# Kernel optimization log

Measured on AMD Instinct MI355X. Metric: run time of the kernel, lower is better.

## Reference

```python
import jax, jax.numpy as jnp
import numpy as np

B, S, D, H, HD = 2, 2048, 768, 12, 64


def setup_inputs() -> dict:
    key = jax.random.key(0)
    ks = jax.random.split(key, 8)
    w = lambda k, shp: jax.random.normal(k, shp, dtype=jnp.float32) * 0.02
    return {
        "hidden_states": jax.random.normal(ks[0], (B, S, D), dtype=jnp.float32),
        "Wq": w(ks[1], (D, D)), "bq": jnp.zeros((D,), jnp.float32),
        "Wk": w(ks[2], (D, D)), "bk": jnp.zeros((D,), jnp.float32),
        "Wv": w(ks[3], (D, D)), "bv": jnp.zeros((D,), jnp.float32),
        # hedgehog feature maps are initialized to identity in the module
        "Wfq": jnp.eye(HD, dtype=jnp.float32) + w(ks[4], (HD, HD)),
        "bfq": jnp.zeros((HD,), jnp.float32),
        "Wfk": jnp.eye(HD, dtype=jnp.float32) + w(ks[5], (HD, HD)),
        "bfk": jnp.zeros((HD,), jnp.float32),
    }


def _heads(x):
    # [B,S,D] -> [B,H,S,HD]
    return x.reshape(B, S, H, HD).transpose(0, 2, 1, 3)


def _feature_map(x, Wf, bf):
    # exp / exp(-x) hedgehog map: [B,H,S,HD] -> [B,H,S,2*HD]
    y = jnp.einsum('bhsd,ed->bhse', x, Wf) + bf
    return jnp.concatenate([jnp.exp(y), jnp.exp(-y)], axis=-1)


def reference(hidden_states, Wq, bq, Wk, bk, Wv, bv, Wfq, bfq, Wfk, bfk):
    h = hidden_states
    q = _heads(h @ Wq.T + bq)   # [B,H,S,HD]
    k = _heads(h @ Wk.T + bk)
    v = _heads(h @ Wv.T + bv)

    # frozen base (softmax) attention producing outputs + true_attns
    scale = 1.0 / np.sqrt(HD).astype(np.float32)
    scores = jnp.einsum('bhmd,bhnd->bhmn', q, k) * scale
    true_attns = jax.nn.softmax(scores, axis=-1)
    out = jnp.einsum('bhmn,bhnd->bhmd', true_attns, v)
    outputs = out.transpose(0, 2, 1, 3).reshape(B, S, D)

    # hedgehog predicted attention: quadratic linear attention
    fq = _feature_map(q, Wfq, bfq)  # [B,H,S,2*HD]
    fk = _feature_map(k, Wfk, bfk)
    qk = jnp.einsum('bhmd,bhnd->bhmn', fq, fk)
    pred_attns = qk / qk.sum(axis=-1, keepdims=True)

    return outputs, pred_attns, true_attns
```

## Files before the change

kernel.cpp:

```cpp
#include <hip/hip_runtime.h>
#include <math.h>

namespace {

constexpr int kB = 2, kS = 2048, kD = 768, kH = 12, kHD = 64, kF = 128, kBH = kB * kH;

typedef __attribute__((ext_vector_type(8))) short short8;
typedef __attribute__((ext_vector_type(4))) short short4v;
typedef __attribute__((ext_vector_type(4))) float f32x4;

__device__ __forceinline__ ushort f2bf(float x) {
    union { float f; unsigned u; } v; v.f = x;
    return (ushort)((v.u + 0x7fffu + ((v.u >> 16) & 1u)) >> 16);
}
__device__ __forceinline__ float bf2f(ushort u) {
    union { unsigned u; float f; } v; v.u = ((unsigned)u) << 16; return v.f;
}

__device__ __forceinline__ void gload16(const ushort* g, void* lds) {
    __builtin_amdgcn_global_load_lds(
        (const __attribute__((address_space(1))) void*)g,
        (__attribute__((address_space(3))) void*)lds, 16, 0, 0);
}

__device__ __forceinline__ void gstage64x64(ushort* ldsBase, const ushort* g,
                                            size_t strideElems, int w, int lane) {
    #pragma unroll
    for (int j = 0; j < 2; ++j) {
        const int row = 16 * w + 8 * j + (lane >> 3);
        const int chunk = lane & 7;
        const ushort* gp = g + (size_t)row * strideElems + ((chunk ^ (row & 7)) * 8);
        void* lp = (char*)ldsBase + (16 * w + 8 * j) * 128;
        gload16(gp, lp);
    }
}
__device__ __forceinline__ void gstageA128(ushort* ldsBase, const ushort* g,
                                           size_t strideElems, int w, int lane) {
    #pragma unroll
    for (int j = 0; j < 4; ++j) {
        const int row = 32 * w + 8 * j + (lane >> 3);
        const int chunk = lane & 7;
        const ushort* gp = g + (size_t)row * strideElems + ((chunk ^ (row & 7)) * 8);
        void* lp = (char*)ldsBase + (32 * w + 8 * j) * 128;
        gload16(gp, lp);
    }
}

__device__ __forceinline__ void gstage8x64(ushort* ldsBase, const ushort* g,
                                           size_t strideElems, int w, int lane) {
    const int row = 8 * w + (lane >> 3);
    const int chunk = lane & 7;
    gload16(g + (size_t)row * strideElems + ((chunk ^ (row & 7)) * 8),
            (char*)ldsBase + 8 * w * 128);
}
__device__ __forceinline__ void gstage8x128(ushort* ldsBase, const ushort* g,
                                            int w, int lane) {
    #pragma unroll
    for (int j = 0; j < 2; ++j) {
        const int row = 8 * w + 4 * j + (lane >> 4);
        const int chunk = lane & 15;
        gload16(g + (size_t)row * kF + ((chunk ^ (row & 7)) * 8),
                (char*)ldsBase + (8 * w + 4 * j) * 256);
    }
}

__global__ __launch_bounds__(256) void cast_kernel(
    const float* __restrict__ s0, const float* __restrict__ s1,
    const float* __restrict__ s2, const float* __restrict__ s3,
    ushort* __restrict__ d0, ushort* __restrict__ d1,
    ushort* __restrict__ d2, ushort* __restrict__ d3)
{
    const int seg = blockIdx.y;
    const float* src = seg == 0 ? s0 : seg == 1 ? s1 : seg == 2 ? s2 : s3;
    ushort* dst      = seg == 0 ? d0 : seg == 1 ? d1 : seg == 2 ? d2 : d3;
    const int n4 = (seg == 0 ? kB * kS * kD : kD * kD) / 4;
    for (int i = blockIdx.x * 256 + threadIdx.x; i < n4; i += gridDim.x * 256) {
        float4 v = *(const float4*)&src[(size_t)i * 4];
        short4v o;
        o[0] = (short)f2bf(v.x); o[1] = (short)f2bf(v.y);
        o[2] = (short)f2bf(v.z); o[3] = (short)f2bf(v.w);
        *(short4v*)&dst[(size_t)i * 4] = o;
    }
}

__global__ __launch_bounds__(256) void qkv_mfma_kernel(
    const ushort* __restrict__ hb,
    const ushort* __restrict__ Wqb, const ushort* __restrict__ Wkb,
    const ushort* __restrict__ Wvb,
    const float* __restrict__ bq, const float* __restrict__ bk,
    const float* __restrict__ bv,
    const float* __restrict__ Wfq, const float* __restrict__ bfq,
    const float* __restrict__ Wfk, const float* __restrict__ bfk,
    ushort* __restrict__ qd, ushort* __restrict__ kd, ushort* __restrict__ vTd,
    ushort* __restrict__ fqd, ushort* __restrict__ fkd,
    float* __restrict__ part)
{
    const int which = blockIdx.z;
    const ushort* __restrict__ Wb  = which == 0 ? Wqb : which == 1 ? Wkb : Wvb;
    const float* __restrict__ bias = which == 0 ? bq : which == 1 ? bk : bv;

    const int m0 = blockIdx.x * 128;
    const int n0 = blockIdx.y * 64;
    const int t = threadIdx.x, lane = t & 63, w = t >> 6;
    const int g = lane >> 4, ln = lane & 15;

    __shared__ __align__(16) ushort As[128 * 64];
    __shared__ __align__(16) ushort Bs[64 * 64];
    __shared__ __align__(16) ushort Ws[64 * 64];
    __shared__ float zsum[4][128];

    if (which < 2) {
        const float* __restrict__ Wf = (which == 0) ? Wfq : Wfk;
        const int row = t >> 2, ce = (t & 3) * 16;
        ushort tmp[16];
        #pragma unroll
        for (int c = 0; c < 16; c += 4) {
            float4 u = *(const float4*)&Wf[(size_t)row * 64 + ce + c];
            tmp[c + 0] = f2bf(u.x); tmp[c + 1] = f2bf(u.y);
            tmp[c + 2] = f2bf(u.z); tmp[c + 3] = f2bf(u.w);
        }
        const int sw = (row & 7) << 4;
        *(uint4*)((char*)Ws + row * 128 + ((ce * 2) ^ sw)) = *(uint4*)&tmp[0];
        *(uint4*)((char*)Ws + row * 128 + ((ce * 2 + 16) ^ sw)) = *(uint4*)&tmp[8];
    }

    f32x4 acc[2][4];
    #pragma unroll
    for (int rs = 0; rs < 2; ++rs)
        #pragma unroll
        for (int nt = 0; nt < 4; ++nt) acc[rs][nt] = (f32x4){0.f, 0.f, 0.f, 0.f};

    for (int k0 = 0; k0 < kD; k0 += 64) {
        gstageA128(As, hb + (size_t)m0 * kD + k0, kD, w, lane);
        gstage64x64(Bs, Wb + (size_t)n0 * kD + k0, kD, w, lane);
        asm volatile("s_waitcnt vmcnt(0)" ::: "memory");
        __builtin_amdgcn_sched_barrier(0);
        __builtin_amdgcn_s_barrier();

        short8 a[2][2], b[4][2];
        #pragma unroll
        for (int rs = 0; rs < 2; ++rs) {
            const int row = 32 * w + 16 * rs + ln, sw = (row & 7) << 4;
            #pragma unroll
            for (int kc = 0; kc < 2; ++kc)
                a[rs][kc] = *(const short8*)((const char*)As + row * 128 + ((kc * 64 + g * 16) ^ sw));
        }
        #pragma unroll
        for (int nt = 0; nt < 4; ++nt) {
            const int rk = nt * 16 + ln, sw = (rk & 7) << 4;
            #pragma unroll
            for (int kc = 0; kc < 2; ++kc)
                b[nt][kc] = *(const short8*)((const char*)Bs + rk * 128 + ((kc * 64 + g * 16) ^ sw));
        }
        #pragma unroll
        for (int rs = 0; rs < 2; ++rs)
            #pragma unroll
            for (int nt = 0; nt < 4; ++nt)
                #pragma unroll
                for (int kc = 0; kc < 2; ++kc)
                    acc[rs][nt] = __builtin_amdgcn_mfma_f32_16x16x32_bf16(
                        a[rs][kc], b[nt][kc], acc[rs][nt], 0, 0, 0);
        asm volatile("s_waitcnt lgkmcnt(0)" ::: "memory");
        __builtin_amdgcn_sched_barrier(0);
        __builtin_amdgcn_s_barrier();
    }

    const int hh = n0 >> 6;
    float bvn[4];
    #pragma unroll
    for (int nt = 0; nt < 4; ++nt) bvn[nt] = bias[n0 + nt * 16 + ln];

    if (which < 2) {
        ushort* __restrict__ dst = (which == 0) ? qd : kd;
        #pragma unroll
        for (int rs = 0; rs < 2; ++rs)
            #pragma unroll
            for (int nt = 0; nt < 4; ++nt)
                #pragma unroll
                for (int r = 0; r < 4; ++r) {
                    const int m = m0 + 32 * w + 16 * rs + g * 4 + r;
                    const int b_ = m >> 11, s_ = m & (kS - 1);
                    dst[((size_t)(b_ * kH + hh) * kS + s_) * kHD + nt * 16 + ln] =
                        f2bf(acc[rs][nt][r] + bvn[nt]);
                }
    } else {
        #pragma unroll
        for (int rs = 0; rs < 2; ++rs)
            #pragma unroll
            for (int nt = 0; nt < 4; ++nt) {
                const int m = m0 + 32 * w + 16 * rs + g * 4;
                const int b_ = m >> 11, s_ = m & (kS - 1);
                const int d = nt * 16 + ln;
                short4v o;
                #pragma unroll
                for (int r = 0; r < 4; ++r) o[r] = (short)f2bf(acc[rs][nt][r] + bvn[nt]);
                *(short4v*)&vTd[((size_t)(b_ * kH + hh) * kHD + d) * kS + s_] = o;
            }
    }

    if (which < 2) {
        __syncthreads();
        #pragma unroll
        for (int rs = 0; rs < 2; ++rs)
            #pragma unroll
            for (int nt = 0; nt < 4; ++nt)
                #pragma unroll
                for (int r = 0; r < 4; ++r) {
                    const int bm = 32 * w + 16 * rs + g * 4 + r;
                    const int e = nt * 16 + ln;
                    *(ushort*)((char*)As + bm * 128 + ((2 * e) ^ ((bm & 7) << 4))) =
                        f2bf(acc[rs][nt][r] + bvn[nt]);
                }
        __syncthreads();

        short8 a2[2][2], b2[4][2];
        #pragma unroll
        for (int rs = 0; rs < 2; ++rs) {
            const int row = 32 * w + 16 * rs + ln, sw = (row & 7) << 4;
            #pragma unroll
            for (int kc = 0; kc < 2; ++kc)
                a2[rs][kc] = *(const short8*)((const char*)As + row * 128 + ((kc * 64 + g * 16) ^ sw));
        }
        #pragma unroll
        for (int nt = 0; nt < 4; ++nt) {
            const int rk = nt * 16 + ln, sw = (rk & 7) << 4;
            #pragma unroll
            for (int kc = 0; kc < 2; ++kc)
                b2[nt][kc] = *(const short8*)((const char*)Ws + rk * 128 + ((kc * 64 + g * 16) ^ sw));
        }
        f32x4 yac[2][4];
        #pragma unroll
        for (int rs = 0; rs < 2; ++rs)
            #pragma unroll
            for (int nt = 0; nt < 4; ++nt) {
                yac[rs][nt] = (f32x4){0.f, 0.f, 0.f, 0.f};
                #pragma unroll
                for (int kc = 0; kc < 2; ++kc)
                    yac[rs][nt] = __builtin_amdgcn_mfma_f32_16x16x32_bf16(
                        a2[rs][kc], b2[nt][kc], yac[rs][nt], 0, 0, 0);
            }

        const float* __restrict__ bf2p = (which == 0) ? bfq : bfk;
        float bfv[4];
        #pragma unroll
        for (int nt = 0; nt < 4; ++nt) bfv[nt] = bf2p[nt * 16 + ln];

        ushort* __restrict__ dstF = (which == 0) ? fqd : fkd;
        float csp[4] = {0.f, 0.f, 0.f, 0.f}, csm[4] = {0.f, 0.f, 0.f, 0.f};
        #pragma unroll
        for (int rs = 0; rs < 2; ++rs)
            #pragma unroll
            for (int nt = 0; nt < 4; ++nt)
                #pragma unroll
                for (int r = 0; r < 4; ++r) {
                    const int m = m0 + 32 * w + 16 * rs + g * 4 + r;
                    const int b_ = m >> 11, s_ = m & (kS - 1);
                    const float y = yac[rs][nt][r] + bfv[nt];
                    const ushort hp = f2bf(__expf(y));
                    const ushort hm = f2bf(__expf(-y));
                    const size_t base =
                        ((size_t)(b_ * kH + hh) * kS + s_) * kF + nt * 16 + ln;
                    dstF[base] = hp;
                    dstF[base + 64] = hm;
                    if (which == 1) { csp[nt] += bf2f(hp); csm[nt] += bf2f(hm); }
                }

        if (which == 1) {
            #pragma unroll
            for (int nt = 0; nt < 4; ++nt) {
                csp[nt] += __shfl_xor(csp[nt], 16); csp[nt] += __shfl_xor(csp[nt], 32);
                csm[nt] += __shfl_xor(csm[nt], 16); csm[nt] += __shfl_xor(csm[nt], 32);
            }
            if (g == 0) {
                #pragma unroll
                for (int nt = 0; nt < 4; ++nt) {
                    zsum[w][nt * 16 + ln]      = csp[nt];
                    zsum[w][64 + nt * 16 + ln] = csm[nt];
                }
            }
            __syncthreads();
            if (t < 128) {
                const float s = zsum[0][t] + zsum[1][t] + zsum[2][t] + zsum[3][t];
                const int b_ = m0 >> 11, gr = (m0 & (kS - 1)) >> 7;
                part[((size_t)((b_ * kH + hh) * 16 + gr)) * kF + t] = s;
            }
        }
    }
}

__global__ __launch_bounds__(512) void true_attn_kernel(
    const ushort* __restrict__ q, const ushort* __restrict__ k,
    const ushort* __restrict__ vT,
    float* __restrict__ out0, float* __restrict__ out2)
{
    const int orig = blockIdx.y * 32 + blockIdx.x;
    const int swz  = (orig & 7) * 96 + (orig >> 3);
    const int bh = swz >> 5, m0 = (swz & 31) * 64;

    const int t = threadIdx.x, lane = t & 63, w = t >> 6;
    const int g = lane >> 4, ln = lane & 15;
    const int wr = w & 3, wc = w >> 2;

    __shared__ __align__(16) ushort Qs[64 * 64];
    __shared__ __align__(16) ushort KVs[4 * 64 * 64];
    __shared__ __align__(16) ushort Ps[64 * 64];
    __shared__ float zl[8][16];

    const ushort* __restrict__ qb = q  + (size_t)bh * kS * kHD;
    const ushort* __restrict__ kb = k  + (size_t)bh * kS * kHD;
    const ushort* __restrict__ vb = vT + (size_t)bh * kHD * kS;

    {
        const int row = t >> 3, ce = (t & 7) * 8;
        uint4 u = *(const uint4*)(qb + (size_t)(m0 + row) * kHD + ce);
        *(uint4*)((char*)Qs + row * 128 + ((ce * 2) ^ ((row & 7) << 4))) = u;
    }
    __syncthreads();

    short8 aq[2];
    {
        const int row = 16 * wr + ln, sw = (row & 7) << 4;
        #pragma unroll
        for (int kc = 0; kc < 2; ++kc)
            aq[kc] = *(const short8*)((const char*)Qs + row * 128 + ((kc * 64 + g * 16) ^ sw));
    }

    gstage8x64(KVs, kb, kHD, w, lane);
    gstage8x64(KVs + 4096, kb + (size_t)64 * kHD, kHD, w, lane);
    float zacc[4] = {0.f, 0.f, 0.f, 0.f};
    for (int tt = 0; tt < 32; ++tt) {
        if (tt + 2 < 32) {
            gstage8x64(KVs + ((tt + 2) & 3) * 4096,
                       kb + (size_t)(tt + 2) * 64 * kHD, kHD, w, lane);
            asm volatile("s_waitcnt vmcnt(2)" ::: "memory");
        } else if (tt == 30) {
            asm volatile("s_waitcnt vmcnt(1)" ::: "memory");
        } else {
            asm volatile("s_waitcnt vmcnt(0)" ::: "memory");
        }
        __builtin_amdgcn_sched_barrier(0);
        __builtin_amdgcn_s_barrier();
        const ushort* KsC = KVs + (tt & 3) * 4096;
        #pragma unroll
        for (int h2 = 0; h2 < 2; ++h2) {
            const int nt = 2 * wc + h2;
            f32x4 c = {0.f, 0.f, 0.f, 0.f};
            const int rk = nt * 16 + ln, sw = (rk & 7) << 4;
            #pragma unroll
            for (int kc = 0; kc < 2; ++kc) {
                short8 b = *(const short8*)((const char*)KsC + rk * 128 + ((kc * 64 + g * 16) ^ sw));
                c = __builtin_amdgcn_mfma_f32_16x16x32_bf16(aq[kc], b, c, 0, 0, 0);
            }
            #pragma unroll
            for (int r = 0; r < 4; ++r) zacc[r] += __expf(c[r] * 0.125f);
        }
    }
    #pragma unroll
    for (int r = 0; r < 4; ++r) {
        float z = zacc[r];
        z += __shfl_xor(z, 1); z += __shfl_xor(z, 2);
        z += __shfl_xor(z, 4); z += __shfl_xor(z, 8);
        zacc[r] = z;
    }
    if (ln == 0) {
        #pragma unroll
        for (int r = 0; r < 4; ++r) zl[w][g * 4 + r] = zacc[r];
    }
    __syncthreads();
    float invl[4];
    #pragma unroll
    for (int r = 0; r < 4; ++r)
        invl[r] = 1.f / (zl[wr][g * 4 + r] + zl[4 + wr][g * 4 + r]);

    f32x4 accv[2];
    accv[0] = (f32x4){0.f, 0.f, 0.f, 0.f};
    accv[1] = (f32x4){0.f, 0.f, 0.f, 0.f};

    gstage8x64(KVs, kb, kHD, w, lane);
    gstage8x64(KVs + 2 * 4096, vb, kS, w, lane);
    for (int tt = 0; tt < 32; ++tt) {
        const int cur = tt & 1;
        const int n0 = tt * 64;
        if (tt + 1 < 32) {
            gstage8x64(KVs + (cur ^ 1) * 4096,
                       kb + (size_t)(tt + 1) * 64 * kHD, kHD, w, lane);
            gstage8x64(KVs + (2 + (cur ^ 1)) * 4096,
                       vb + (tt + 1) * 64, kS, w, lane);
            asm volatile("s_waitcnt vmcnt(2)" ::: "memory");
        } else {
            asm volatile("s_waitcnt vmcnt(0)" ::: "memory");
        }
        __builtin_amdgcn_sched_barrier(0);
        __builtin_amdgcn_s_barrier();

        const ushort* KsC = KVs + cur * 4096;
        const ushort* VsC = KVs + (2 + cur) * 4096;
        #pragma unroll
        for (int h2 = 0; h2 < 2; ++h2) {
            const int nt = 2 * wc + h2;
            f32x4 c = {0.f, 0.f, 0.f, 0.f};
            const int rk = nt * 16 + ln, sw = (rk & 7) << 4;
            #pragma unroll
            for (int kc = 0; kc < 2; ++kc) {
                short8 b = *(const short8*)((const char*)KsC + rk * 128 + ((kc * 64 + g * 16) ^ sw));
                c = __builtin_amdgcn_mfma_f32_16x16x32_bf16(aq[kc], b, c, 0, 0, 0);
            }
            #pragma unroll
            for (int r = 0; r < 4; ++r) {
                const int prow = 16 * wr + g * 4 + r;
                const float p = __expf(c[r] * 0.125f) * invl[r];
                out2[((size_t)bh * kS + m0 + prow) * kS + n0 + nt * 16 + ln] = p;
                const int pb = prow * 128 + ((2 * (nt * 16 + ln)) ^ ((prow & 7) << 4));
                *(ushort*)((char*)Ps + pb) = f2bf(p);
            }
        }
        asm volatile("s_waitcnt lgkmcnt(0)" ::: "memory");
        __builtin_amdgcn_sched_barrier(0);
        __builtin_amdgcn_s_barrier();

        const int rowp = 16 * wr + ln, swp = (rowp & 7) << 4;
        #pragma unroll
        for (int kc = 0; kc < 2; ++kc) {
            short8 pa = *(const short8*)((const char*)Ps + rowp * 128 + ((kc * 64 + g * 16) ^ swp));
            #pragma unroll
            for (int d2 = 0; d2 < 2; ++d2) {
                const int dt = 2 * wc + d2;
                const int rv = dt * 16 + ln, swv = (rv & 7) << 4;
                short8 bv = *(const short8*)((const char*)VsC + rv * 128 + ((kc * 64 + g * 16) ^ swv));
                accv[d2] = __builtin_amdgcn_mfma_f32_16x16x32_bf16(pa, bv, accv[d2], 0, 0, 0);
            }
        }
        __builtin_amdgcn_sched_barrier(0);
        __builtin_amdgcn_s_barrier();
    }

    const int b_ = bh / kH, h_ = bh % kH;
    #pragma unroll
    for (int d2 = 0; d2 < 2; ++d2)
        #pragma unroll
        for (int r = 0; r < 4; ++r) {
            const int prow = 16 * wr + g * 4 + r;
            const int dt = 2 * wc + d2;
            out0[((size_t)b_ * kS + m0 + prow) * kD + h_ * kHD + dt * 16 + ln] = accv[d2][r];
        }
}

__global__ __launch_bounds__(512) void pred_attn_kernel(
    const ushort* __restrict__ fq, const ushort* __restrict__ fk,
    const float* __restrict__ part, float* __restrict__ out1)
{
    const int orig = blockIdx.y * 32 + blockIdx.x;
    const int swz  = (orig & 7) * 96 + (orig >> 3);
    const int bh = swz >> 5, m0 = (swz & 31) * 64;

    const int t = threadIdx.x, lane = t & 63, w = t >> 6;
    const int g = lane >> 4, ln = lane & 15;
    const int wr = w & 3, wc = w >> 2;

    __shared__ __align__(16) ushort Fq[64 * 128];
    __shared__ __align__(16) ushort Fk[2 * 64 * 128];
    __shared__ float fsum[128];
    __shared__ float invz[64];

    const ushort* __restrict__ fqb = fq + (size_t)bh * kS * kF;
    const ushort* __restrict__ fkb = fk + (size_t)bh * kS * kF;

    {
        const int row = t >> 3, ce = (t & 7) * 16;
        const ushort* s = fqb + (size_t)(m0 + row) * kF + ce;
        const int sw = (row & 7) << 4;
        *(uint4*)((char*)Fq + row * 256 + ((ce * 2) ^ sw)) = *(const uint4*)s;
        *(uint4*)((char*)Fq + row * 256 + ((ce * 2 + 16) ^ sw)) = *(const uint4*)(s + 8);
    }
    if (t < 128) {
        float s = 0.f;
        #pragma unroll
        for (int gg = 0; gg < 16; ++gg) s += part[((size_t)bh * 16 + gg) * kF + t];
        fsum[t] = s;
    }
    __syncthreads();

    short8 a[4];
    {
        const int row = 16 * wr + ln, sw = (row & 7) << 4;
        #pragma unroll
        for (int kc = 0; kc < 4; ++kc)
            a[kc] = *(const short8*)((const char*)Fq + row * 256 + ((kc * 64 + g * 16) ^ sw));
    }

    float den = 0.f;
    #pragma unroll
    for (int kc = 0; kc < 4; ++kc)
        #pragma unroll
        for (int j = 0; j < 8; ++j)
            den += bf2f((ushort)a[kc][j]) * fsum[kc * 32 + g * 8 + j];
    den += __shfl_xor(den, 16);
    den += __shfl_xor(den, 32);
    if (g == 0) invz[16 * wr + ln] = 1.f / den;
    __syncthreads();
    float invl[4];
    #pragma unroll
    for (int r = 0; r < 4; ++r) invl[r] = invz[16 * wr + g * 4 + r];

    gstage8x128(Fk, fkb, w, lane);
    for (int tt = 0; tt < 32; ++tt) {
        const int cur = tt & 1;
        const int n0 = tt * 64;
        if (tt + 1 < 32) {
            gstage8x128(Fk + (cur ^ 1) * 8192, fkb + (size_t)(tt + 1) * 64 * kF, w, lane);
            asm volatile("s_waitcnt vmcnt(2)" ::: "memory");
        } else {
            asm volatile("s_waitcnt vmcnt(0)" ::: "memory");
        }
        __builtin_amdgcn_sched_barrier(0);
        __builtin_amdgcn_s_barrier();

        const ushort* FkC = Fk + cur * 8192;
        #pragma unroll
        for (int h2 = 0; h2 < 2; ++h2) {
            const int nt = 2 * wc + h2;
            f32x4 c = {0.f, 0.f, 0.f, 0.f};
            const int rk = nt * 16 + ln, sw = (rk & 7) << 4;
            #pragma unroll
            for (int kc = 0; kc < 4; ++kc) {
                short8 b = *(const short8*)((const char*)FkC + rk * 256 + ((kc * 64 + g * 16) ^ sw));
                c = __builtin_amdgcn_mfma_f32_16x16x32_bf16(a[kc], b, c, 0, 0, 0);
            }
            #pragma unroll
            for (int r = 0; r < 4; ++r)
                out1[((size_t)bh * kS + m0 + 16 * wr + g * 4 + r) * kS + n0 + nt * 16 + ln] =
                    c[r] * invl[r];
        }
        __builtin_amdgcn_sched_barrier(0);
        __builtin_amdgcn_s_barrier();
    }
}

}

extern "C" void kernel_launch(void* const* d_in, const int* in_sizes, int n_in,
                              void* d_out, int out_size, void* d_ws, size_t ws_size,
                              hipStream_t stream)
{
    (void)in_sizes; (void)n_in; (void)out_size; (void)ws_size;

    const float* hidden = (const float*)d_in[0];
    const float* Wq = (const float*)d_in[1];
    const float* bq = (const float*)d_in[2];
    const float* Wk = (const float*)d_in[3];
    const float* bk = (const float*)d_in[4];
    const float* Wv = (const float*)d_in[5];
    const float* bv = (const float*)d_in[6];
    const float* Wfq = (const float*)d_in[7];
    const float* bfq = (const float*)d_in[8];
    const float* Wfk = (const float*)d_in[9];
    const float* bfk = (const float*)d_in[10];

    float* out = (float*)d_out;
    float* out0 = out;
    float* out1 = out0 + (size_t)kB * kS * kD;
    float* out2 = out1 + (size_t)kBH * kS * kS;

    float* part = (float*)d_ws;
    ushort* hb  = (ushort*)(part + (size_t)kBH * 16 * kF);
    ushort* Wqb = hb  + (size_t)kB * kS * kD;
    ushort* Wkb = Wqb + (size_t)kD * kD;
    ushort* Wvb = Wkb + (size_t)kD * kD;
    ushort* qw  = Wvb + (size_t)kD * kD;
    ushort* kw  = qw  + (size_t)kBH * kS * kHD;
    ushort* vTw = kw  + (size_t)kBH * kS * kHD;
    ushort* fqw = vTw + (size_t)kBH * kS * kHD;
    ushort* fkw = fqw + (size_t)kBH * kS * kF;

    cast_kernel<<<dim3(512, 4), 256, 0, stream>>>(
        hidden, Wq, Wk, Wv, hb, Wqb, Wkb, Wvb);
    qkv_mfma_kernel<<<dim3(kB * kS / 128, kD / 64, 3), 256, 0, stream>>>(
        hb, Wqb, Wkb, Wvb, bq, bk, bv,
        Wfq, bfq, Wfk, bfk,
        qw, kw, vTw, fqw, fkw, part);
    true_attn_kernel<<<dim3(kS / 64, kBH), 512, 0, stream>>>(qw, kw, vTw, out0, out2);
    pred_attn_kernel<<<dim3(kS / 64, kBH), 512, 0, stream>>>(fqw, fkw, part, out1);
}
```

Measured before the change: 301.0 us.

## Alias LDS buffers and split pred-attention key range across two blocks

In true_attn, the Q staging buffer and the P tile now share one LDS array. In pred_attn, the Fq tile and the double-buffered Fk tiles also share one array. This cuts shared memory per block so more blocks can be resident on a CU. pred_attn also splits each query tile's key range into two halves, handled by separate blocks with a reworked swizzled 1D grid. That doubles the block count and halves per-block loop length, but each block repeats the Fq load and the normaliser computation.

```diff
diff --git a/kernel.cpp b/kernel.cpp
--- a/kernel.cpp
+++ b/kernel.cpp
@@ -301,9 +301,8 @@
     const int g = lane >> 4, ln = lane & 15;
     const int wr = w & 3, wc = w >> 2;
 
-    __shared__ __align__(16) ushort Qs[64 * 64];
+    __shared__ __align__(16) ushort QPs[64 * 64];
     __shared__ __align__(16) ushort KVs[4 * 64 * 64];
-    __shared__ __align__(16) ushort Ps[64 * 64];
     __shared__ float zl[8][16];
 
     const ushort* __restrict__ qb = q  + (size_t)bh * kS * kHD;
@@ -313,7 +312,7 @@
     {
         const int row = t >> 3, ce = (t & 7) * 8;
         uint4 u = *(const uint4*)(qb + (size_t)(m0 + row) * kHD + ce);
-        *(uint4*)((char*)Qs + row * 128 + ((ce * 2) ^ ((row & 7) << 4))) = u;
+        *(uint4*)((char*)QPs + row * 128 + ((ce * 2) ^ ((row & 7) << 4))) = u;
     }
     __syncthreads();
 
@@ -322,7 +321,7 @@
         const int row = 16 * wr + ln, sw = (row & 7) << 4;
         #pragma unroll
         for (int kc = 0; kc < 2; ++kc)
-            aq[kc] = *(const short8*)((const char*)Qs + row * 128 + ((kc * 64 + g * 16) ^ sw));
+            aq[kc] = *(const short8*)((const char*)QPs + row * 128 + ((kc * 64 + g * 16) ^ sw));
     }
 
     gstage8x64(KVs, kb, kHD, w, lane);
@@ -411,7 +410,7 @@
                 const float p = __expf(c[r] * 0.125f) * invl[r];
                 out2[((size_t)bh * kS + m0 + prow) * kS + n0 + nt * 16 + ln] = p;
                 const int pb = prow * 128 + ((2 * (nt * 16 + ln)) ^ ((prow & 7) << 4));
-                *(ushort*)((char*)Ps + pb) = f2bf(p);
+                *(ushort*)((char*)QPs + pb) = f2bf(p);
             }
         }
         asm volatile("s_waitcnt lgkmcnt(0)" ::: "memory");
@@ -421,7 +420,7 @@
         const int rowp = 16 * wr + ln, swp = (rowp & 7) << 4;
         #pragma unroll
         for (int kc = 0; kc < 2; ++kc) {
-            short8 pa = *(const short8*)((const char*)Ps + rowp * 128 + ((kc * 64 + g * 16) ^ swp));
+            short8 pa = *(const short8*)((const char*)QPs + rowp * 128 + ((kc * 64 + g * 16) ^ swp));
             #pragma unroll
             for (int d2 = 0; d2 < 2; ++d2) {
                 const int dt = 2 * wc + d2;
@@ -449,16 +448,15 @@
     const ushort* __restrict__ fq, const ushort* __restrict__ fk,
     const float* __restrict__ part, float* __restrict__ out1)
 {
-    const int orig = blockIdx.y * 32 + blockIdx.x;
-    const int swz  = (orig & 7) * 96 + (orig >> 3);
-    const int bh = swz >> 5, m0 = (swz & 31) * 64;
+    const int orig = blockIdx.x;
+    const int idx  = (orig & 7) * 192 + (orig >> 3);
+    const int bh = idx >> 6, m0 = ((idx & 63) >> 1) * 64, nhalf = idx & 1;
 
     const int t = threadIdx.x, lane = t & 63, w = t >> 6;
     const int g = lane >> 4, ln = lane & 15;
     const int wr = w & 3, wc = w >> 2;
 
-    __shared__ __align__(16) ushort Fq[64 * 128];
-    __shared__ __align__(16) ushort Fk[2 * 64 * 128];
+    __shared__ __align__(16) ushort sbuf[2 * 64 * 128];
     __shared__ float fsum[128];
     __shared__ float invz[64];
 
@@ -469,8 +467,8 @@
         const int row = t >> 3, ce = (t & 7) * 16;
         const ushort* s = fqb + (size_t)(m0 + row) * kF + ce;
         const int sw = (row & 7) << 4;
-        *(uint4*)((char*)Fq + row * 256 + ((ce * 2) ^ sw)) = *(const uint4*)s;
-        *(uint4*)((char*)Fq + row * 256 + ((ce * 2 + 16) ^ sw)) = *(const uint4*)(s + 8);
+        *(uint4*)((char*)sbuf + row * 256 + ((ce * 2) ^ sw)) = *(const uint4*)s;
+        *(uint4*)((char*)sbuf + row * 256 + ((ce * 2 + 16) ^ sw)) = *(const uint4*)(s + 8);
     }
     if (t < 128) {
         float s = 0.f;
@@ -485,7 +483,7 @@
         const int row = 16 * wr + ln, sw = (row & 7) << 4;
         #pragma unroll
         for (int kc = 0; kc < 4; ++kc)
-            a[kc] = *(const short8*)((const char*)Fq + row * 256 + ((kc * 64 + g * 16) ^ sw));
+            a[kc] = *(const short8*)((const char*)sbuf + row * 256 + ((kc * 64 + g * 16) ^ sw));
     }
 
     float den = 0.f;
@@ -502,12 +500,14 @@
     #pragma unroll
     for (int r = 0; r < 4; ++r) invl[r] = invz[16 * wr + g * 4 + r];
 
-    gstage8x128(Fk, fkb, w, lane);
-    for (int tt = 0; tt < 32; ++tt) {
+    const int t0 = nhalf * 16;
+    gstage8x128(sbuf, fkb + (size_t)t0 * 64 * kF, w, lane);
+    for (int tt = 0; tt < 16; ++tt) {
         const int cur = tt & 1;
-        const int n0 = tt * 64;
-        if (tt + 1 < 32) {
-            gstage8x128(Fk + (cur ^ 1) * 8192, fkb + (size_t)(tt + 1) * 64 * kF, w, lane);
+        const int n0 = (t0 + tt) * 64;
+        if (tt + 1 < 16) {
+            gstage8x128(sbuf + (cur ^ 1) * 8192,
+                        fkb + (size_t)(t0 + tt + 1) * 64 * kF, w, lane);
             asm volatile("s_waitcnt vmcnt(2)" ::: "memory");
         } else {
             asm volatile("s_waitcnt vmcnt(0)" ::: "memory");
@@ -515,7 +515,7 @@
         __builtin_amdgcn_sched_barrier(0);
         __builtin_amdgcn_s_barrier();
 
-        const ushort* FkC = Fk + cur * 8192;
+        const ushort* FkC = sbuf + cur * 8192;
         #pragma unroll
         for (int h2 = 0; h2 < 2; ++h2) {
             const int nt = 2 * wc + h2;
@@ -579,5 +579,6 @@
         Wfq, bfq, Wfk, bfk,
         qw, kw, vTw, fqw, fkw, part);
     true_attn_kernel<<<dim3(kS / 64, kBH), 512, 0, stream>>>(qw, kw, vTw, out0, out2);
-    pred_attn_kernel<<<dim3(kS / 64, kBH), 512, 0, stream>>>(fqw, fkw, part, out1);
-}
+    pred_attn_kernel<<<dim3(2 * kS / 64 * kBH / 2 * 2), 512, 0, stream>>>(
+        fqw, fkw, part, out1);
+}
```

Result: faster. 293.5 us (median of 2 runs) (-2.5%).
